# Optimization experiments

Hardware: AMD Instinct MI355X
Metric: run time of the kernel (lower is better)

Reference implementation:

```python
import jax, jax.numpy as jnp
import numpy as np

MEMORY_SIZE = 512
EMBED_DIM = 768
BATCH, SEQ = 4, 8192


def setup_inputs() -> dict:
    key = jax.random.key(0)
    k1, k2 = jax.random.split(key)
    hidden_states = jax.random.normal(k1, (BATCH, SEQ, EMBED_DIM), dtype=jnp.float32)
    memory = jax.random.normal(k2, (MEMORY_SIZE, EMBED_DIM), dtype=jnp.float32)
    return {"hidden_states": hidden_states, "memory": memory}


def reference(hidden_states, memory):
    # importance[s] = mean over batch of L2 norm of hidden_states[b, s, :]
    importance = jnp.linalg.norm(hidden_states, axis=-1).mean(axis=0)  # [S]
    k = min(MEMORY_SIZE, importance.shape[0])  # static
    _, topk_idx = jax.lax.top_k(importance, k)  # [k]
    # gather per-token batch-mean vectors and scatter into first k memory slots
    mean_h = hidden_states.mean(axis=0)  # [S, D]
    new_memory = memory.at[:k].set(mean_h[topk_idx])  # [M, D]
    return new_memory
```

## Files before the change

kernel.cpp:

```cpp
#include <hip/hip_runtime.h>
#include <stdint.h>

#define S_TOK 8192
#define D_DIM 768
#define B_SZ  4
#define K_TOP 512

__global__ __launch_bounds__(256) void importance_kernel(const float4* __restrict__ h4,
                                                         float* __restrict__ imp) {
    const int D4 = D_DIM / 4;
    int wave = (blockIdx.x * blockDim.x + threadIdx.x) >> 6;
    int lane = threadIdx.x & 63;
    if (wave >= S_TOK) return;
    float acc = 0.f;
#pragma unroll
    for (int b = 0; b < B_SZ; ++b) {
        const float4* row = h4 + ((size_t)b * S_TOK + (size_t)wave) * D4;
        float ss = 0.f;
#pragma unroll
        for (int j = 0; j < 3; ++j) {
            float4 v = row[lane + 64 * j];
            ss += v.x * v.x + v.y * v.y + v.z * v.z + v.w * v.w;
        }
#pragma unroll
        for (int off = 32; off >= 1; off >>= 1) ss += __shfl_xor(ss, off);
        acc += sqrtf(ss);
    }
    if (lane == 0) imp[wave] = acc * 0.25f;
}

__global__ __launch_bounds__(1024) void topk_kernel(const float* __restrict__ imp,
                                                    int* __restrict__ topk) {
    const int NT = 1024;
    const int tid = threadIdx.x;
    const int lane = tid & 63;
    const int wid = tid >> 6;
    __shared__ uint32_t s_keys[S_TOK];
    __shared__ uint32_t s_hist[256];
    __shared__ uint32_t s_wsum[16];
    __shared__ unsigned long long s_sel[K_TOP];
    __shared__ uint32_t s_prefix, s_want, s_cntgt;

    for (int i = tid; i < S_TOK; i += NT) s_keys[i] = __float_as_uint(imp[i]);
    if (tid == 0) { s_prefix = 0u; s_want = K_TOP; s_cntgt = 0u; }
    __syncthreads();

    uint32_t dmask = 0u;
    for (int shift = 24; shift >= 0; shift -= 8) {
        if (tid < 256) s_hist[tid] = 0u;
        __syncthreads();
        const uint32_t pfx = s_prefix;
        const uint32_t want_in = s_want;
        for (int i = tid; i < S_TOK; i += NT) {
            uint32_t k = s_keys[i];
            if ((k & dmask) == pfx) atomicAdd(&s_hist[(k >> shift) & 0xFFu], 1u);
        }
        __syncthreads();
        if (wid == 0) {
            uint32_t c0 = s_hist[4 * lane + 0];
            uint32_t c1 = s_hist[4 * lane + 1];
            uint32_t c2 = s_hist[4 * lane + 2];
            uint32_t c3 = s_hist[4 * lane + 3];
            uint32_t ls = c0 + c1 + c2 + c3;
            uint32_t s = ls;
            for (int off = 1; off < 64; off <<= 1) {
                uint32_t v = __shfl_down(s, off);
                if (lane + off < 64) s += v;
            }
            uint32_t above = s - ls;
            uint32_t sstr3 = above;
            uint32_t sstr2 = sstr3 + c3;
            uint32_t sstr1 = sstr2 + c2;
            uint32_t sstr0 = sstr1 + c1;
            const uint32_t w = want_in;
            int b = -1; uint32_t nw = 0;
            if      (sstr3 < w && w <= sstr3 + c3) { b = 4 * lane + 3; nw = w - sstr3; }
            else if (sstr2 < w && w <= sstr2 + c2) { b = 4 * lane + 2; nw = w - sstr2; }
            else if (sstr1 < w && w <= sstr1 + c1) { b = 4 * lane + 1; nw = w - sstr1; }
            else if (sstr0 < w && w <= sstr0 + c0) { b = 4 * lane + 0; nw = w - sstr0; }
            if (b >= 0) {
                s_prefix = pfx | ((uint32_t)b << shift);
                s_want = nw;
            }
        }
        dmask |= (0xFFu << shift);
        __syncthreads();
    }
    const uint32_t T = s_prefix;
    const uint32_t need_eq = s_want;

    for (int i = tid; i < S_TOK; i += NT) {
        uint32_t k = s_keys[i];
        if (k > T) {
            uint32_t p = atomicAdd(&s_cntgt, 1u);
            s_sel[p] = ((unsigned long long)k << 32) | (uint32_t)(~(uint32_t)i);
        }
    }
    __syncthreads();
    const uint32_t cntgt = s_cntgt;

    const int PER = S_TOK / NT;
    const int my0 = tid * PER;
    uint32_t loc = 0;
#pragma unroll
    for (int j = 0; j < PER; ++j) loc += (s_keys[my0 + j] == T) ? 1u : 0u;
    uint32_t incl = loc;
    for (int off = 1; off < 64; off <<= 1) {
        uint32_t v = __shfl_up(incl, off);
        if (lane >= off) incl += v;
    }
    if (lane == 63) s_wsum[wid] = incl;
    __syncthreads();
    uint32_t wbase = 0;
    for (int wj = 0; wj < wid; ++wj) wbase += s_wsum[wj];
    uint32_t rank = wbase + incl - loc;
#pragma unroll
    for (int j = 0; j < PER; ++j) {
        if (s_keys[my0 + j] == T) {
            if (rank < need_eq)
                s_sel[cntgt + rank] =
                    ((unsigned long long)T << 32) | (uint32_t)(~(uint32_t)(my0 + j));
            ++rank;
        }
    }
    __syncthreads();

    if (tid < K_TOP) {
        const unsigned long long a = s_sel[tid];
        uint32_t r = 0;
        for (int j = 0; j < K_TOP; ++j) r += (s_sel[j] > a) ? 1u : 0u;
        topk[r] = (int)(~(uint32_t)(a & 0xFFFFFFFFull));
    }
}

__global__ __launch_bounds__(192) void gather_kernel(const float4* __restrict__ h4,
                                                     const int* __restrict__ topk,
                                                     float4* __restrict__ out4) {
    const int D4 = D_DIM / 4;
    const size_t SD4 = (size_t)S_TOK * D4;
    int row = blockIdx.x;
    int idx = topk[row];
    const float4* base = h4 + (size_t)idx * D4;
    int d = threadIdx.x;
    float4 a = base[d];
    float4 b = base[d + SD4];
    float4 c = base[d + 2 * SD4];
    float4 e = base[d + 3 * SD4];
    float4 r;
    r.x = 0.25f * (a.x + b.x + c.x + e.x);
    r.y = 0.25f * (a.y + b.y + c.y + e.y);
    r.z = 0.25f * (a.z + b.z + c.z + e.z);
    r.w = 0.25f * (a.w + b.w + c.w + e.w);
    out4[(size_t)row * D4 + d] = r;
}

extern "C" void kernel_launch(void* const* d_in, const int* in_sizes, int n_in,
                              void* d_out, int out_size, void* d_ws, size_t ws_size,
                              hipStream_t stream) {
    const float* h = (const float*)d_in[0];
    float* out = (float*)d_out;
    float* imp = (float*)d_ws;
    int* topk = (int*)((char*)d_ws + S_TOK * sizeof(float));

    importance_kernel<<<S_TOK / 4, 256, 0, stream>>>((const float4*)h, imp);
    topk_kernel<<<1, 1024, 0, stream>>>(imp, topk);
    gather_kernel<<<K_TOP, 192, 0, stream>>>((const float4*)h, topk, (float4*)out);
}
```

Measured before the change: 46.09 us.

## Fuse top-k selection into gather with per-block rank selection

Replaces the single-block top-k plus separate gather with one kernel of 512 blocks. Each block redundantly radix-selects the key whose rank equals its blockIdx (ties broken by lower index) and then gathers and averages that token row. Histograms become per-wave and use wave-aggregated updates. This removes the serial single-block sort stage and one launch, at the cost of 512 blocks each redoing the full 8192-key radix pass over shared memory.

```diff
diff --git a/kernel.cpp b/kernel.cpp
--- a/kernel.cpp
+++ b/kernel.cpp
@@ -29,38 +29,66 @@
     if (lane == 0) imp[wave] = acc * 0.25f;
 }
 
-__global__ __launch_bounds__(1024) void topk_kernel(const float* __restrict__ imp,
-                                                    int* __restrict__ topk) {
-    const int NT = 1024;
+__global__ __launch_bounds__(512) void select_gather_kernel(const float* __restrict__ imp,
+                                                            const float4* __restrict__ h4,
+                                                            float4* __restrict__ out4) {
+    const int NT = 512;
     const int tid = threadIdx.x;
     const int lane = tid & 63;
     const int wid = tid >> 6;
     __shared__ uint32_t s_keys[S_TOK];
-    __shared__ uint32_t s_hist[256];
-    __shared__ uint32_t s_wsum[16];
-    __shared__ unsigned long long s_sel[K_TOP];
-    __shared__ uint32_t s_prefix, s_want, s_cntgt;
+    __shared__ uint32_t s_hist[8][256];
+    __shared__ uint32_t s_red[8];
+    __shared__ uint32_t s_prefix, s_want;
+    __shared__ int s_idx;
 
-    for (int i = tid; i < S_TOK; i += NT) s_keys[i] = __float_as_uint(imp[i]);
-    if (tid == 0) { s_prefix = 0u; s_want = K_TOP; s_cntgt = 0u; }
+    const uint4* imp4 = (const uint4*)imp;
+#pragma unroll
+    for (int k = 0; k < 4; ++k) {
+        uint4 v = imp4[tid + k * NT];
+        ((uint4*)s_keys)[tid + k * NT] = v;
+    }
+    if (tid == 0) { s_prefix = 0u; s_want = (uint32_t)blockIdx.x + 1u; s_idx = 0; }
     __syncthreads();
 
     uint32_t dmask = 0u;
     for (int shift = 24; shift >= 0; shift -= 8) {
-        if (tid < 256) s_hist[tid] = 0u;
+        ((uint4*)s_hist)[tid] = make_uint4(0u, 0u, 0u, 0u);
         __syncthreads();
         const uint32_t pfx = s_prefix;
         const uint32_t want_in = s_want;
-        for (int i = tid; i < S_TOK; i += NT) {
-            uint32_t k = s_keys[i];
-            if ((k & dmask) == pfx) atomicAdd(&s_hist[(k >> shift) & 0xFFu], 1u);
+        uint32_t* mh = s_hist[wid];
+#pragma unroll
+        for (int k = 0; k < 4; ++k) {
+            uint4 kv = ((const uint4*)s_keys)[tid + k * NT];
+            uint32_t ks[4] = {kv.x, kv.y, kv.z, kv.w};
+#pragma unroll
+            for (int j = 0; j < 4; ++j) {
+                uint32_t key = ks[j];
+                bool active = ((key & dmask) == pfx);
+                uint32_t bin = (key >> shift) & 0xFFu;
+                unsigned long long act = __ballot(active);
+                if (act) {
+                    int fl = __ffsll(act) - 1;
+                    uint32_t b0 = __shfl(bin, fl);
+                    unsigned long long same = __ballot(active && (bin == b0));
+                    if (same == act) {
+                        if (lane == fl) mh[b0] += (uint32_t)__popcll(act);
+                    } else if (active) {
+                        atomicAdd(&mh[bin], 1u);
+                    }
+                }
+            }
         }
         __syncthreads();
         if (wid == 0) {
-            uint32_t c0 = s_hist[4 * lane + 0];
-            uint32_t c1 = s_hist[4 * lane + 1];
-            uint32_t c2 = s_hist[4 * lane + 2];
-            uint32_t c3 = s_hist[4 * lane + 3];
+            uint4 a = make_uint4(0u, 0u, 0u, 0u);
+#pragma unroll
+            for (int w = 0; w < 8; ++w) {
+                uint4 v = ((const uint4*)(s_hist[w]))[lane];
+                a.x += v.x; a.y += v.y; a.z += v.z; a.w += v.w;
+            }
+            uint32_t c0 = a.x, c1 = a.y, c2 = a.z, c3 = a.w;
             uint32_t ls = c0 + c1 + c2 + c3;
             uint32_t s = ls;
             for (int off = 1; off < 64; off <<= 1) {
@@ -87,71 +115,55 @@
         __syncthreads();
     }
     const uint32_t T = s_prefix;
-    const uint32_t need_eq = s_want;
+    const uint32_t need = s_want;
 
-    for (int i = tid; i < S_TOK; i += NT) {
-        uint32_t k = s_keys[i];
-        if (k > T) {
-            uint32_t p = atomicAdd(&s_cntgt, 1u);
-            s_sel[p] = ((unsigned long long)k << 32) | (uint32_t)(~(uint32_t)i);
-        }
+    const int my0 = tid * 16;
+    uint32_t kk[16];
+#pragma unroll
+    for (int jj = 0; jj < 4; ++jj) {
+        int j = (jj + (lane >> 1)) & 3;
+        uint4 v = ((const uint4*)s_keys)[tid * 4 + j];
+        kk[4 * j + 0] = v.x; kk[4 * j + 1] = v.y;
+        kk[4 * j + 2] = v.z; kk[4 * j + 3] = v.w;
     }
-    __syncthreads();
-    const uint32_t cntgt = s_cntgt;
-
-    const int PER = S_TOK / NT;
-    const int my0 = tid * PER;
-    uint32_t loc = 0;
+    uint32_t cnt = 0;
 #pragma unroll
-    for (int j = 0; j < PER; ++j) loc += (s_keys[my0 + j] == T) ? 1u : 0u;
-    uint32_t incl = loc;
+    for (int j = 0; j < 16; ++j) cnt += (kk[j] == T) ? 1u : 0u;
+    uint32_t incl = cnt;
     for (int off = 1; off < 64; off <<= 1) {
         uint32_t v = __shfl_up(incl, off);
         if (lane >= off) incl += v;
     }
-    if (lane == 63) s_wsum[wid] = incl;
+    if (lane == 63) s_red[wid] = incl;
     __syncthreads();
     uint32_t wbase = 0;
-    for (int wj = 0; wj < wid; ++wj) wbase += s_wsum[wj];
-    uint32_t rank = wbase + incl - loc;
+    for (int wj = 0; wj < wid; ++wj) wbase += s_red[wj];
+    uint32_t p = wbase + incl - cnt;
 #pragma unroll
-    for (int j = 0; j < PER; ++j) {
-        if (s_keys[my0 + j] == T) {
-            if (rank < need_eq)
-                s_sel[cntgt + rank] =
-                    ((unsigned long long)T << 32) | (uint32_t)(~(uint32_t)(my0 + j));
-            ++rank;
+    for (int j = 0; j < 16; ++j) {
+        if (kk[j] == T) {
+            ++p;
+            if (p == need) s_idx = my0 + j;
         }
     }
     __syncthreads();
 
-    if (tid < K_TOP) {
-        const unsigned long long a = s_sel[tid];
-        uint32_t r = 0;
-        for (int j = 0; j < K_TOP; ++j) r += (s_sel[j] > a) ? 1u : 0u;
-        topk[r] = (int)(~(uint32_t)(a & 0xFFFFFFFFull));
+    const int idx = s_idx;
+    if (tid < D_DIM / 4) {
+        const int D4 = D_DIM / 4;
+        const size_t SD4 = (size_t)S_TOK * D4;
+        const float4* base = h4 + (size_t)idx * D4;
+        float4 a = base[tid];
+        float4 b = base[tid + SD4];
+        float4 c = base[tid + 2 * SD4];
+        float4 e = base[tid + 3 * SD4];
+        float4 r;
+        r.x = 0.25f * (a.x + b.x + c.x + e.x);
+        r.y = 0.25f * (a.y + b.y + c.y + e.y);
+        r.z = 0.25f * (a.z + b.z + c.z + e.z);
+        r.w = 0.25f * (a.w + b.w + c.w + e.w);
+        out4[(size_t)blockIdx.x * D4 + tid] = r;
     }
-}
-
-__global__ __launch_bounds__(192) void gather_kernel(const float4* __restrict__ h4,
-                                                     const int* __restrict__ topk,
-                                                     float4* __restrict__ out4) {
-    const int D4 = D_DIM / 4;
-    const size_t SD4 = (size_t)S_TOK * D4;
-    int row = blockIdx.x;
-    int idx = topk[row];
-    const float4* base = h4 + (size_t)idx * D4;
-    int d = threadIdx.x;
-    float4 a = base[d];
-    float4 b = base[d + SD4];
-    float4 c = base[d + 2 * SD4];
-    float4 e = base[d + 3 * SD4];
-    float4 r;
-    r.x = 0.25f * (a.x + b.x + c.x + e.x);
-    r.y = 0.25f * (a.y + b.y + c.y + e.y);
-    r.z = 0.25f * (a.z + b.z + c.z + e.z);
-    r.w = 0.25f * (a.w + b.w + c.w + e.w);
-    out4[(size_t)row * D4 + d] = r;
 }
 
 extern "C" void kernel_launch(void* const* d_in, const int* in_sizes, int n_in,
@@ -160,9 +172,7 @@
     const float* h = (const float*)d_in[0];
     float* out = (float*)d_out;
     float* imp = (float*)d_ws;
-    int* topk = (int*)((char*)d_ws + S_TOK * sizeof(float));
 
     importance_kernel<<<S_TOK / 4, 256, 0, stream>>>((const float4*)h, imp);
-    topk_kernel<<<1, 1024, 0, stream>>>(imp, topk);
-    gather_kernel<<<K_TOP, 192, 0, stream>>>((const float4*)h, topk, (float4*)out);
+    select_gather_kernel<<<K_TOP, 512, 0, stream>>>(imp, (const float4*)h, (float4*)out);
 }
```

New measurement: 39.55 us. 14.2% less time.
